# Kernel optimization log

Measured on AMD Instinct MI355X. Metric: run time of the kernel, lower is better.

The kernel has to match this reference:

```python
import jax, jax.numpy as jnp
import numpy as np

B, S, D, H = 2, 2048, 1024, 16
HD = D // H               # head_dim = input_size / num_heads
STEPS = 1                 # update_steps_max extra Hopfield update steps
LN_EPS = 1e-5
SCALING = 1.0 / np.sqrt(HD)  # beta = 1/sqrt(head_dim)


def layernorm(x, g, b):
    m = x.mean(-1, keepdims=True)
    v = ((x - m) ** 2).mean(-1, keepdims=True)
    return (x - m) * jax.lax.rsqrt(v + LN_EPS) * g + b


def setup_inputs() -> dict:
    key = jax.random.key(0)
    ks = jax.random.split(key, 9)
    s = 0.02
    f32 = jnp.float32
    return {
        "data": jax.random.normal(ks[0], (B, S, D), f32),
        # affine LayerNorm params (stored / state / projection patterns)
        "g_k": jnp.ones((D,), f32), "b_k": jnp.zeros((D,), f32),
        "g_q": jnp.ones((D,), f32), "b_q": jnp.zeros((D,), f32),
        "g_v": jnp.ones((D,), f32), "b_v": jnp.zeros((D,), f32),
        # in-projections (q/k/v) and out-projection of HopfieldCore
        "Wq": jax.random.normal(ks[1], (D, D), f32) * s, "bq": jnp.zeros((D,), f32),
        "Wk": jax.random.normal(ks[2], (D, D), f32) * s, "bk": jnp.zeros((D,), f32),
        "Wv": jax.random.normal(ks[3], (D, D), f32) * s, "bv": jnp.zeros((D,), f32),
        "Wo": jax.random.normal(ks[4], (D, D), f32) * s, "bo": jnp.zeros((D,), f32),
    }


def reference(data, g_k, b_k, g_q, b_q, g_v, b_v,
              Wq, bq, Wk, bk, Wv, bv, Wo, bo):
    # single input tensor used as stored / state / projection pattern
    xk = layernorm(data, g_k, b_k)   # stored pattern  -> keys
    xq = layernorm(data, g_q, b_q)   # state pattern   -> queries
    xv = layernorm(data, g_v, b_v)   # pattern proj    -> values

    split = lambda t: t.reshape(B, S, H, HD).transpose(0, 2, 1, 3)  # [B,H,S,HD]
    q = split(xq @ Wq + bq)
    k = split(xk @ Wk + bk)
    v = split(xv @ Wv + bv)

    def assoc(q):  # xi = softmax(beta * q K^T)
        return jax.nn.softmax(
            jnp.einsum('bhqd,bhkd->bhqk', q, k) * SCALING, axis=-1)

    xi = assoc(q)
    for _ in range(STEPS):           # iterative Hopfield update: q <- xi K
        q = jnp.einsum('bhqk,bhkd->bhqd', xi, k)
        xi = assoc(q)

    out = jnp.einsum('bhqk,bhkd->bhqd', xi, v)        # retrieve with values
    out = out.transpose(0, 2, 1, 3).reshape(B, S, D)  # merge heads
    return out @ Wo + bo
```

## Files before the change

kernel.cpp:

```cpp
#include <hip/hip_runtime.h>
#include <hip/hip_bf16.h>

#define B_  2
#define S_  2048
#define D_  1024
#define H_  16
#define HD_ 64
#define M_  4096


typedef __attribute__((ext_vector_type(8))) short short8;
typedef __attribute__((ext_vector_type(4))) float f32x4;

#define CE_ 0.1803368801111204f
#define SD_ 56

static __device__ __forceinline__ unsigned short f2bfc(float f){
  union{float f; unsigned u;} c; c.f = f;
  return (unsigned short)((c.u + 0x8000u) >> 16);
}
static __device__ __forceinline__ unsigned pk2bf(float a, float b){
  union{float f; unsigned u;} ca, cb; ca.f=a; cb.f=b;
  return __builtin_amdgcn_perm(cb.u + 0x8000u, ca.u + 0x8000u, 0x07060302u);
}
static __device__ __forceinline__ unsigned pk2bft(float a, float b){
  union{float f; unsigned u;} ca, cb; ca.f=a; cb.f=b;
  return __builtin_amdgcn_perm(cb.u, ca.u, 0x07060302u);
}

__global__ __launch_bounds__(256) void stats_kernel(const float* __restrict__ x,
                                                    float* __restrict__ mean,
                                                    float* __restrict__ rstd){
  int row = blockIdx.x*4 + (threadIdx.x>>6);
  int l = threadIdx.x & 63;
  const float4* xr = (const float4*)(x + (size_t)row*D_);
  float s = 0.f, ss = 0.f;
  #pragma unroll
  for (int i=0;i<4;i++){
    float4 v = xr[l + 64*i];
    s  += v.x+v.y+v.z+v.w;
    ss += v.x*v.x+v.y*v.y+v.z*v.z+v.w*v.w;
  }
  #pragma unroll
  for (int m=1;m<64;m<<=1){ s += __shfl_xor(s, m, 64); ss += __shfl_xor(ss, m, 64); }
  if (l==0){
    float me = s*(1.0f/D_);
    float var = ss*(1.0f/D_) - me*me;
    mean[row] = me;
    rstd[row] = rsqrtf(var + 1e-5f);
  }
}

__global__ __launch_bounds__(256) void biasfold_kernel(
  const float* __restrict__ Wq, const float* __restrict__ Wk, const float* __restrict__ Wv,
  const float* __restrict__ blq, const float* __restrict__ blk, const float* __restrict__ blv,
  const float* __restrict__ bpq, const float* __restrict__ bpk, const float* __restrict__ bpv,
  float* __restrict__ bf){
  int z = blockIdx.y;
  const float* W  = (z==0)?Wq:(z==1)?Wk:Wv;
  const float* bl = (z==0)?blq:(z==1)?blk:blv;
  const float* bp = (z==0)?bpq:(z==1)?bpk:bpv;
  int nl = threadIdx.x & 63, kg = threadIdx.x >> 6;
  int n = blockIdx.x*64 + nl;
  float acc = 0.f;
  for (int k = kg*256; k < (kg+1)*256; k++)
    acc += bl[k] * W[(size_t)k*D_ + n];
  __shared__ float red[4][64];
  red[kg][nl] = acc;
  __syncthreads();
  if (threadIdx.x < 64){
    int nn = blockIdx.x*64 + threadIdx.x;
    float v = red[0][threadIdx.x]+red[1][threadIdx.x]+red[2][threadIdx.x]+red[3][threadIdx.x]
              + bp[nn];
    bf[z*D_ + nn] = (z==0) ? v*CE_ : v;
  }
}

__global__ __launch_bounds__(256) void wtrans_kernel(
  const float* __restrict__ Wq, const float* __restrict__ Wk,
  const float* __restrict__ Wv, const float* __restrict__ Wo,
  const float* __restrict__ gq, const float* __restrict__ gk,
  const float* __restrict__ gv,
  unsigned short* __restrict__ WT){
  int z = blockIdx.z;
  const float* W = (z==0)?Wq:(z==1)?Wk:(z==2)?Wv:Wo;
  const float* g = (z==0)?gq:(z==1)?gk:(z==2)?gv:(const float*)0;
  unsigned short* out = WT + ((size_t)z<<20);
  int k0 = blockIdx.x*64, n0 = blockIdx.y*64;
  __shared__ unsigned short tile[64][72];
  int t = threadIdx.x;
  {
    int kr = t>>2, c16 = (t&3)*16;
    float gs = g ? g[k0+kr]*((z==0)?CE_:1.0f) : 1.0f;
    const float* src = W + (size_t)(k0+kr)*D_ + n0 + c16;
    float4 w0 = *(const float4*)(src);
    float4 w1 = *(const float4*)(src+4);
    float4 w2 = *(const float4*)(src+8);
    float4 w3 = *(const float4*)(src+12);
    unsigned* tp = (unsigned*)&tile[kr][c16];
    tp[0]=pk2bf(w0.x*gs,w0.y*gs); tp[1]=pk2bf(w0.z*gs,w0.w*gs);
    tp[2]=pk2bf(w1.x*gs,w1.y*gs); tp[3]=pk2bf(w1.z*gs,w1.w*gs);
    tp[4]=pk2bf(w2.x*gs,w2.y*gs); tp[5]=pk2bf(w2.z*gs,w2.w*gs);
    tp[6]=pk2bf(w3.x*gs,w3.y*gs); tp[7]=pk2bf(w3.z*gs,w3.w*gs);
  }
  __syncthreads();
  {
    int nr = t>>2, kc = (t&3)*16;
    union { uint4 v[2]; unsigned short u[16]; } st;
    #pragma unroll
    for (int i=0;i<16;i++) st.u[i] = tile[kc+i][nr];
    unsigned short* dst = out + (size_t)(n0+nr)*D_ + k0 + kc;
    *(uint4*)(dst)     = st.v[0];
    *(uint4*)(dst + 8) = st.v[1];
  }
}

__global__ __launch_bounds__(256) void gemm_qkv(
  const float* __restrict__ data,
  const unsigned short* __restrict__ WT,
  const float* __restrict__ biasf,
  const float* __restrict__ mean, const float* __restrict__ rstd,
  unsigned short* __restrict__ qv, unsigned short* __restrict__ kb,
  unsigned short* __restrict__ kT, unsigned short* __restrict__ vT)
{
  int z = blockIdx.z;
  const unsigned short* Bt = WT + ((size_t)z<<20);
  const float* bias = biasf + z*D_;
  unsigned short* oN = (z==0)?qv:(z==1)?kb:(unsigned short*)0;
  unsigned short* oT = (z==0)?(unsigned short*)0:(z==1)?kT:vT;

  __shared__ __align__(16) unsigned short As[128*SD_];
  __shared__ __align__(16) unsigned short Bs[128*SD_];
  int tid = threadIdx.x, w = tid>>6, l = tid&63;
  int m0 = blockIdx.x*128, n0 = blockIdx.y*128;
  int wr = (w>>1)*64, wc = (w&1)*64;
  int lr = l&15, qd = l>>4;
  int srow = tid>>2, scol = (tid&3)*8;

  float rs0 = rstd[m0+srow],    nm0 = -mean[m0+srow]*rs0;
  float rs1 = rstd[m0+srow+64], nm1 = -mean[m0+srow+64]*rs1;

  const f32x4 fz = {0.f,0.f,0.f,0.f};
  f32x4 acc[4][4];
  #pragma unroll
  for (int i=0;i<4;i++)
    #pragma unroll
    for (int j=0;j<4;j++) acc[i][j] = fz;

  for (int kk=0; kk<D_; kk+=32){
    __syncthreads();
    {
      const float* p0 = data + (size_t)(m0+srow   )*D_ + kk + scol;
      const float* p1 = data + (size_t)(m0+srow+64)*D_ + kk + scol;
      float4 a0 = *(const float4*)(p0), a0b = *(const float4*)(p0+4);
      float4 a1 = *(const float4*)(p1), a1b = *(const float4*)(p1+4);
      uint4 o0, o1;
      o0.x = pk2bf(fmaf(a0.x ,rs0,nm0), fmaf(a0.y ,rs0,nm0));
      o0.y = pk2bf(fmaf(a0.z ,rs0,nm0), fmaf(a0.w ,rs0,nm0));
      o0.z = pk2bf(fmaf(a0b.x,rs0,nm0), fmaf(a0b.y,rs0,nm0));
      o0.w = pk2bf(fmaf(a0b.z,rs0,nm0), fmaf(a0b.w,rs0,nm0));
      o1.x = pk2bf(fmaf(a1.x ,rs1,nm1), fmaf(a1.y ,rs1,nm1));
      o1.y = pk2bf(fmaf(a1.z ,rs1,nm1), fmaf(a1.w ,rs1,nm1));
      o1.z = pk2bf(fmaf(a1b.x,rs1,nm1), fmaf(a1b.y,rs1,nm1));
      o1.w = pk2bf(fmaf(a1b.z,rs1,nm1), fmaf(a1b.w,rs1,nm1));
      *(uint4*)(As + srow*SD_      + scol) = o0;
      *(uint4*)(As + (srow+64)*SD_ + scol) = o1;
    }
    *(uint4*)(Bs + srow*SD_      + scol) = *(const uint4*)(Bt + (size_t)(n0+srow   )*D_ + kk + scol);
    *(uint4*)(Bs + (srow+64)*SD_ + scol) = *(const uint4*)(Bt + (size_t)(n0+srow+64)*D_ + kk + scol);
    __syncthreads();
    short8 af[4], bfr[4];
    #pragma unroll
    for (int i=0;i<4;i++) af[i]  = *(const short8*)(As + (wr + i*16 + lr)*SD_ + qd*8);
    #pragma unroll
    for (int j=0;j<4;j++) bfr[j] = *(const short8*)(Bs + (wc + j*16 + lr)*SD_ + qd*8);
    #pragma unroll
    for (int i=0;i<4;i++)
      #pragma unroll
      for (int j=0;j<4;j++)
        acc[i][j] = __builtin_amdgcn_mfma_f32_16x16x32_bf16(af[i], bfr[j], acc[i][j], 0, 0, 0);
  }

  #pragma unroll
  for (int j=0;j<4;j++){
    int n = n0 + wc + j*16 + lr;
    float bias_n = bias[n];
    #pragma unroll
    for (int i=0;i<4;i++){
      int mb = m0 + wr + i*16 + qd*4;
      float v0 = acc[i][j][0] + bias_n;
      float v1 = acc[i][j][1] + bias_n;
      float v2 = acc[i][j][2] + bias_n;
      float v3 = acc[i][j][3] + bias_n;
      if (oN){
        oN[(size_t)(mb+0)*D_ + n] = f2bfc(v0);
        oN[(size_t)(mb+1)*D_ + n] = f2bfc(v1);
        oN[(size_t)(mb+2)*D_ + n] = f2bfc(v2);
        oN[(size_t)(mb+3)*D_ + n] = f2bfc(v3);
      }
      if (oT){
        int bb = mb >> 11, sI = mb & (S_-1);
        int hh = n >> 6,  dd = n & 63;
        uint2 pk; pk.x = pk2bf(v0, v1); pk.y = pk2bf(v2, v3);
        *(uint2*)(oT + (size_t)((bb*H_ + hh)*HD_ + dd)*S_ + sI) = pk;
      }
    }
  }
}

__global__ __launch_bounds__(256) void gemm_out(
  const unsigned short* __restrict__ A,
  const unsigned short* __restrict__ Bt,
  const float* __restrict__ bo,
  float* __restrict__ Cf)
{
  __shared__ __align__(16) unsigned short As[128*SD_];
  __shared__ __align__(16) unsigned short Bs[128*SD_];
  int tid = threadIdx.x, w = tid>>6, l = tid&63;
  int m0 = blockIdx.x*128, n0 = blockIdx.y*128;
  int wr = (w>>1)*64, wc = (w&1)*64;
  int lr = l&15, qd = l>>4;
  int srow = tid>>2, scol = (tid&3)*8;

  const f32x4 fz = {0.f,0.f,0.f,0.f};
  f32x4 acc[4][4];
  #pragma unroll
  for (int i=0;i<4;i++)
    #pragma unroll
    for (int j=0;j<4;j++) acc[i][j] = fz;

  for (int kk=0; kk<D_; kk+=32){
    __syncthreads();
    *(uint4*)(As + srow*SD_      + scol) = *(const uint4*)(A  + (size_t)(m0+srow   )*D_ + kk + scol);
    *(uint4*)(As + (srow+64)*SD_ + scol) = *(const uint4*)(A  + (size_t)(m0+srow+64)*D_ + kk + scol);
    *(uint4*)(Bs + srow*SD_      + scol) = *(const uint4*)(Bt + (size_t)(n0+srow   )*D_ + kk + scol);
    *(uint4*)(Bs + (srow+64)*SD_ + scol) = *(const uint4*)(Bt + (size_t)(n0+srow+64)*D_ + kk + scol);
    __syncthreads();
    short8 af[4], bfr[4];
    #pragma unroll
    for (int i=0;i<4;i++) af[i]  = *(const short8*)(As + (wr + i*16 + lr)*SD_ + qd*8);
    #pragma unroll
    for (int j=0;j<4;j++) bfr[j] = *(const short8*)(Bs + (wc + j*16 + lr)*SD_ + qd*8);
    #pragma unroll
    for (int i=0;i<4;i++)
      #pragma unroll
      for (int j=0;j<4;j++)
        acc[i][j] = __builtin_amdgcn_mfma_f32_16x16x32_bf16(af[i], bfr[j], acc[i][j], 0, 0, 0);
  }

  #pragma unroll
  for (int j=0;j<4;j++){
    int n = n0 + wc + j*16 + lr;
    float bias_n = bo[n];
    #pragma unroll
    for (int i=0;i<4;i++){
      int mb = m0 + wr + i*16 + qd*4;
      Cf[(size_t)(mb+0)*D_ + n] = acc[i][j][0] + bias_n;
      Cf[(size_t)(mb+1)*D_ + n] = acc[i][j][1] + bias_n;
      Cf[(size_t)(mb+2)*D_ + n] = acc[i][j][2] + bias_n;
      Cf[(size_t)(mb+3)*D_ + n] = acc[i][j][3] + bias_n;
    }
  }
}

__global__ __launch_bounds__(256) void attn_fused(
  unsigned short* __restrict__ QO,
  const unsigned short* __restrict__ K,
  const unsigned short* __restrict__ KT,
  const unsigned short* __restrict__ VT)
{
  int qt = blockIdx.x;
  int h  = blockIdx.y;
  int b  = qt >> 4;
  int bh = b*H_ + h;
  int tid = threadIdx.x, w = tid>>6, l = tid&63;
  int lr = l&15, qd = l>>4;
  int r8 = tid>>3, c8 = (tid&7)*8;
  int chf = c8>>5, co = c8&31;

  __shared__ __align__(16) unsigned short sK[2][64*SD_];
  __shared__ __align__(16) unsigned short sV[2][64*SD_];
  __shared__ __align__(16) unsigned short sP[4][2][32*SD_];

  const f32x4 fz = {0.f,0.f,0.f,0.f};

  unsigned short* Qbase = QO + (size_t)(qt*128 + w*32) * D_ + h*64;
  short8 qf[2][2];
  #pragma unroll
  for (int gg=0; gg<2; gg++)
    #pragma unroll
    for (int hf=0; hf<2; hf++)
      qf[gg][hf] = *(const short8*)(Qbase + (size_t)(gg*16+lr)*D_ + hf*32 + qd*8);

  const unsigned short* Khead = K + (size_t)(b*S_)*D_ + h*64;
  const unsigned short* Vh0 = KT + (size_t)bh*HD_*S_;
  const unsigned short* Vh1 = VT + (size_t)bh*HD_*S_;
  unsigned short* Pw0 = &sP[w][0][0];
  unsigned short* Pw1 = &sP[w][1][0];

  f32x4 oacc[2][4];
  float lac[2];

  uint4 kr0, kr1, vr0, vr1;
  {
    kr0 = *(const uint4*)(Khead + (size_t)(r8   )*D_ + c8);
    kr1 = *(const uint4*)(Khead + (size_t)(r8+32)*D_ + c8);
    vr0 = *(const uint4*)(Vh0 + (size_t)(r8   )*S_ + c8);
    vr1 = *(const uint4*)(Vh0 + (size_t)(r8+32)*S_ + c8);
  }

  #pragma unroll 1
  for (int phase=0; phase<2; phase++){
    const unsigned short* Vhead = phase ? Vh1 : Vh0;
    lac[0]=0.f; lac[1]=0.f;
    #pragma unroll
    for (int gg=0;gg<2;gg++)
      #pragma unroll
      for (int t=0;t<4;t++) oacc[gg][t]=fz;

    for (int kt=0; kt<S_; kt+=64){
      __syncthreads();
      *(uint4*)(&sK[chf][(r8   )*SD_ + co]) = kr0;
      *(uint4*)(&sK[chf][(r8+32)*SD_ + co]) = kr1;
      *(uint4*)(&sV[chf][(r8   )*SD_ + co]) = vr0;
      *(uint4*)(&sV[chf][(r8+32)*SD_ + co]) = vr1;
      __syncthreads();

      {
        int nkt = kt + 64;
        const unsigned short* Vn = Vhead;
        if (nkt >= S_){ nkt = 0; Vn = Vh1; }
        kr0 = *(const uint4*)(Khead + (size_t)(nkt+r8   )*D_ + c8);
        kr1 = *(const uint4*)(Khead + (size_t)(nkt+r8+32)*D_ + c8);
        vr0 = *(const uint4*)(Vn + (size_t)(r8   )*S_ + nkt + c8);
        vr1 = *(const uint4*)(Vn + (size_t)(r8+32)*S_ + nkt + c8);
      }

      f32x4 sc[2][4];
      #pragma unroll
      for (int st=0; st<4; st++){
        short8 kA0 = *(const short8*)(&sK[0][(st*16+lr)*SD_ + qd*8]);
        short8 kA1 = *(const short8*)(&sK[1][(st*16+lr)*SD_ + qd*8]);
        #pragma unroll
        for (int gg=0; gg<2; gg++){
          f32x4 z = fz;
          z = __builtin_amdgcn_mfma_f32_16x16x32_bf16(kA0, qf[gg][0], z, 0,0,0);
          z = __builtin_amdgcn_mfma_f32_16x16x32_bf16(kA1, qf[gg][1], z, 0,0,0);
          sc[gg][st] = z;
        }
      }
      #pragma unroll
      for (int gg=0; gg<2; gg++)
        #pragma unroll
        for (int st=0; st<4; st++){
          float p0=__builtin_amdgcn_exp2f(sc[gg][st][0]);
          float p1=__builtin_amdgcn_exp2f(sc[gg][st][1]);
          float p2=__builtin_amdgcn_exp2f(sc[gg][st][2]);
          float p3=__builtin_amdgcn_exp2f(sc[gg][st][3]);
          lac[gg] += (p0+p1)+(p2+p3);
          uint2 pk; pk.x = pk2bft(p0,p1); pk.y = pk2bft(p2,p3);
          unsigned short* Ph = (st&2) ? Pw1 : Pw0;
          *(uint2*)(Ph + (gg*16+lr)*SD_ + (st&1)*16 + qd*4) = pk;
        }
      short8 pf[2][2];
      #pragma unroll
      for (int gg=0; gg<2; gg++){
        pf[gg][0] = *(const short8*)(Pw0 + (gg*16+lr)*SD_ + qd*8);
        pf[gg][1] = *(const short8*)(Pw1 + (gg*16+lr)*SD_ + qd*8);
      }
      #pragma unroll
      for (int dt=0; dt<4; dt++){
        short8 vA0 = *(const short8*)(&sV[0][(dt*16+lr)*SD_ + qd*8]);
        short8 vA1 = *(const short8*)(&sV[1][(dt*16+lr)*SD_ + qd*8]);
        #pragma unroll
        for (int gg=0; gg<2; gg++){
          oacc[gg][dt] = __builtin_amdgcn_mfma_f32_16x16x32_bf16(vA0, pf[gg][0], oacc[gg][dt], 0,0,0);
          oacc[gg][dt] = __builtin_amdgcn_mfma_f32_16x16x32_bf16(vA1, pf[gg][1], oacc[gg][dt], 0,0,0);
        }
      }
    }

    #pragma unroll
    for (int gg=0;gg<2;gg++){
      lac[gg] += __shfl_xor(lac[gg], 16, 64);
      lac[gg] += __shfl_xor(lac[gg], 32, 64);
    }

    if (phase==0){
      #pragma unroll
      for (int gg=0;gg<2;gg++){
        float iv = CE_ * __builtin_amdgcn_rcpf(lac[gg]);
        #pragma unroll
        for (int dt=0;dt<4;dt++){
          uint2 pk;
          pk.x = pk2bf(oacc[gg][dt][0]*iv, oacc[gg][dt][1]*iv);
          pk.y = pk2bf(oacc[gg][dt][2]*iv, oacc[gg][dt][3]*iv);
          unsigned short* Ph = (dt&2) ? Pw1 : Pw0;
          *(uint2*)(Ph + (gg*16+lr)*SD_ + (dt&1)*16 + qd*4) = pk;
        }
      }
      __builtin_amdgcn_s_waitcnt(0);
      #pragma unroll
      for (int gg=0;gg<2;gg++){
        qf[gg][0] = *(const short8*)(Pw0 + (gg*16+lr)*SD_ + qd*8);
        qf[gg][1] = *(const short8*)(Pw1 + (gg*16+lr)*SD_ + qd*8);
      }
    } else {
      #pragma unroll
      for (int gg=0;gg<2;gg++){
        float iv = __builtin_amdgcn_rcpf(lac[gg]);
        unsigned short* Ob = QO + (size_t)(qt*128 + w*32 + gg*16 + lr)*D_ + h*64;
        #pragma unroll
        for (int dt=0;dt<4;dt++){
          uint2 pk;
          pk.x = pk2bf(oacc[gg][dt][0]*iv, oacc[gg][dt][1]*iv);
          pk.y = pk2bf(oacc[gg][dt][2]*iv, oacc[gg][dt][3]*iv);
          *(uint2*)(Ob + dt*16 + qd*4) = pk;
        }
      }
    }
  }
}

extern "C" void kernel_launch(void* const* d_in, const int* in_sizes, int n_in,
                              void* d_out, int out_size, void* d_ws, size_t ws_size,
                              hipStream_t stream){
  const float* data = (const float*)d_in[0];
  const float* g_k  = (const float*)d_in[1];
  const float* b_k  = (const float*)d_in[2];
  const float* g_q  = (const float*)d_in[3];
  const float* b_q  = (const float*)d_in[4];
  const float* g_v  = (const float*)d_in[5];
  const float* b_v  = (const float*)d_in[6];
  const float* Wq   = (const float*)d_in[7];
  const float* bq   = (const float*)d_in[8];
  const float* Wk   = (const float*)d_in[9];
  const float* bk   = (const float*)d_in[10];
  const float* Wv   = (const float*)d_in[11];
  const float* bv   = (const float*)d_in[12];
  const float* Wo   = (const float*)d_in[13];
  const float* bo   = (const float*)d_in[14];
  float* out = (float*)d_out;

  char* ws = (char*)d_ws;
  const size_t MB = (size_t)1<<20;
  unsigned short* q    = (unsigned short*)(ws);
  unsigned short* kb   = (unsigned short*)(ws + 8*MB);
  unsigned short* WT   = (unsigned short*)(ws + 16*MB);
  unsigned short* WTo  = WT + ((size_t)3<<20);
  float*          bfld = (float*)(ws + 24*MB);
  float*          mean = bfld + 3*D_;
  float*          rstd = mean + M_;
  unsigned short* vT   = (unsigned short*)d_out;
  unsigned short* kT   = (unsigned short*)((char*)d_out + 8*MB);

  dim3 gb(256);
  stats_kernel<<<dim3(M_/4), gb, 0, stream>>>(data, mean, rstd);
  biasfold_kernel<<<dim3(16,3), gb, 0, stream>>>(Wq,Wk,Wv, b_q,b_k,b_v, bq,bk,bv, bfld);
  wtrans_kernel<<<dim3(16,16,4), gb, 0, stream>>>(Wq,Wk,Wv,Wo, g_q,g_k,g_v, WT);
  gemm_qkv<<<dim3(32,8,3), gb, 0, stream>>>(data, WT, bfld, mean, rstd, q, kb, kT, vT);
  attn_fused<<<dim3(32, H_), gb, 0, stream>>>(q, kb, kT, vT);
  gemm_out<<<dim3(32,8), gb, 0, stream>>>(q, WTo, bo, out);
}
```

Baseline: 292.4 us.

## Merge prep kernels into one launch and use direct global-to-LDS loads in GEMMs

Three preprocessing kernels (row stats, weight transpose/convert, bias fold) are combined into one launch that dispatches on block index, removing two launch gaps. The QKV and output GEMMs now stage bf16 tiles with global_load_lds (direct global-to-LDS DMA) instead of going through registers, and those tiles use an unpadded 32-element row stride. The unpadded layout may bring back LDS bank conflicts on the fragment reads. The attention kernel, which likely dominates runtime, is not changed.

```diff
diff --git a/kernel.cpp b/kernel.cpp
--- a/kernel.cpp
+++ b/kernel.cpp
@@ -15,6 +15,12 @@
 #define CE_ 0.1803368801111204f
 #define SD_ 56
 
+typedef __attribute__((address_space(1))) const unsigned GU;
+typedef __attribute__((address_space(3))) unsigned LU;
+static __device__ __forceinline__ void glds16(const void* g, void* l){
+  __builtin_amdgcn_global_load_lds((GU*)g, (LU*)l, 16, 0, 0);
+}
+
 static __device__ __forceinline__ unsigned short f2bfc(float f){
   union{float f; unsigned u;} c; c.f = f;
   return (unsigned short)((c.u + 0x8000u) >> 16);
@@ -28,90 +34,86 @@
   return __builtin_amdgcn_perm(cb.u, ca.u, 0x07060302u);
 }
 
-__global__ __launch_bounds__(256) void stats_kernel(const float* __restrict__ x,
-                                                    float* __restrict__ mean,
-                                                    float* __restrict__ rstd){
-  int row = blockIdx.x*4 + (threadIdx.x>>6);
-  int l = threadIdx.x & 63;
-  const float4* xr = (const float4*)(x + (size_t)row*D_);
-  float s = 0.f, ss = 0.f;
-  #pragma unroll
-  for (int i=0;i<4;i++){
-    float4 v = xr[l + 64*i];
-    s  += v.x+v.y+v.z+v.w;
-    ss += v.x*v.x+v.y*v.y+v.z*v.z+v.w*v.w;
-  }
-  #pragma unroll
-  for (int m=1;m<64;m<<=1){ s += __shfl_xor(s, m, 64); ss += __shfl_xor(ss, m, 64); }
-  if (l==0){
-    float me = s*(1.0f/D_);
-    float var = ss*(1.0f/D_) - me*me;
-    mean[row] = me;
-    rstd[row] = rsqrtf(var + 1e-5f);
-  }
-}
-
-__global__ __launch_bounds__(256) void biasfold_kernel(
-  const float* __restrict__ Wq, const float* __restrict__ Wk, const float* __restrict__ Wv,
+__global__ __launch_bounds__(256) void prep_kernel(
+  const float* __restrict__ data, float* __restrict__ mean, float* __restrict__ rstd,
+  const float* __restrict__ Wq, const float* __restrict__ Wk,
+  const float* __restrict__ Wv, const float* __restrict__ Wo,
+  const float* __restrict__ gq, const float* __restrict__ gk, const float* __restrict__ gv,
   const float* __restrict__ blq, const float* __restrict__ blk, const float* __restrict__ blv,
   const float* __restrict__ bpq, const float* __restrict__ bpk, const float* __restrict__ bpv,
-  float* __restrict__ bf){
-  int z = blockIdx.y;
-  const float* W  = (z==0)?Wq:(z==1)?Wk:Wv;
-  const float* bl = (z==0)?blq:(z==1)?blk:blv;
-  const float* bp = (z==0)?bpq:(z==1)?bpk:bpv;
-  int nl = threadIdx.x & 63, kg = threadIdx.x >> 6;
-  int n = blockIdx.x*64 + nl;
-  float acc = 0.f;
-  for (int k = kg*256; k < (kg+1)*256; k++)
-    acc += bl[k] * W[(size_t)k*D_ + n];
+  unsigned short* __restrict__ WT, float* __restrict__ bf)
+{
+  __shared__ unsigned short tile[64][72];
   __shared__ float red[4][64];
-  red[kg][nl] = acc;
-  __syncthreads();
-  if (threadIdx.x < 64){
-    int nn = blockIdx.x*64 + threadIdx.x;
-    float v = red[0][threadIdx.x]+red[1][threadIdx.x]+red[2][threadIdx.x]+red[3][threadIdx.x]
-              + bp[nn];
-    bf[z*D_ + nn] = (z==0) ? v*CE_ : v;
-  }
-}
-
-__global__ __launch_bounds__(256) void wtrans_kernel(
-  const float* __restrict__ Wq, const float* __restrict__ Wk,
-  const float* __restrict__ Wv, const float* __restrict__ Wo,
-  const float* __restrict__ gq, const float* __restrict__ gk,
-  const float* __restrict__ gv,
-  unsigned short* __restrict__ WT){
-  int z = blockIdx.z;
-  const float* W = (z==0)?Wq:(z==1)?Wk:(z==2)?Wv:Wo;
-  const float* g = (z==0)?gq:(z==1)?gk:(z==2)?gv:(const float*)0;
-  unsigned short* out = WT + ((size_t)z<<20);
-  int k0 = blockIdx.x*64, n0 = blockIdx.y*64;
-  __shared__ unsigned short tile[64][72];
-  int t = threadIdx.x;
-  {
-    int kr = t>>2, c16 = (t&3)*16;
-    float gs = g ? g[k0+kr]*((z==0)?CE_:1.0f) : 1.0f;
-    const float* src = W + (size_t)(k0+kr)*D_ + n0 + c16;
-    float4 w0 = *(const float4*)(src);
-    float4 w1 = *(const float4*)(src+4);
-    float4 w2 = *(const float4*)(src+8);
-    float4 w3 = *(const float4*)(src+12);
-    unsigned* tp = (unsigned*)&tile[kr][c16];
-    tp[0]=pk2bf(w0.x*gs,w0.y*gs); tp[1]=pk2bf(w0.z*gs,w0.w*gs);
-    tp[2]=pk2bf(w1.x*gs,w1.y*gs); tp[3]=pk2bf(w1.z*gs,w1.w*gs);
-    tp[4]=pk2bf(w2.x*gs,w2.y*gs); tp[5]=pk2bf(w2.z*gs,w2.w*gs);
-    tp[6]=pk2bf(w3.x*gs,w3.y*gs); tp[7]=pk2bf(w3.z*gs,w3.w*gs);
-  }
-  __syncthreads();
-  {
-    int nr = t>>2, kc = (t&3)*16;
-    union { uint4 v[2]; unsigned short u[16]; } st;
-    #pragma unroll
-    for (int i=0;i<16;i++) st.u[i] = tile[kc+i][nr];
-    unsigned short* dst = out + (size_t)(n0+nr)*D_ + k0 + kc;
-    *(uint4*)(dst)     = st.v[0];
-    *(uint4*)(dst + 8) = st.v[1];
+  int bid = blockIdx.x, t = threadIdx.x;
+  if (bid < 1024){
+    int row = bid*4 + (t>>6);
+    int l = t & 63;
+    const float4* xr = (const float4*)(data + (size_t)row*D_);
+    float s = 0.f, ss = 0.f;
+    #pragma unroll
+    for (int i=0;i<4;i++){
+      float4 v = xr[l + 64*i];
+      s  += v.x+v.y+v.z+v.w;
+      ss += v.x*v.x+v.y*v.y+v.z*v.z+v.w*v.w;
+    }
+    #pragma unroll
+    for (int m=1;m<64;m<<=1){ s += __shfl_xor(s, m, 64); ss += __shfl_xor(ss, m, 64); }
+    if (l==0){
+      float me = s*(1.0f/D_);
+      float var = ss*(1.0f/D_) - me*me;
+      mean[row] = me;
+      rstd[row] = rsqrtf(var + 1e-5f);
+    }
+  } else if (bid < 2048){
+    int idx = bid - 1024;
+    int z = idx >> 8, rem = idx & 255;
+    int k0 = (rem>>4)*64, n0 = (rem&15)*64;
+    const float* W = (z==0)?Wq:(z==1)?Wk:(z==2)?Wv:Wo;
+    const float* g = (z==0)?gq:(z==1)?gk:(z==2)?gv:(const float*)0;
+    unsigned short* out = WT + ((size_t)z<<20);
+    {
+      int kr = t>>2, c16 = (t&3)*16;
+      float gs = g ? g[k0+kr]*((z==0)?CE_:1.0f) : 1.0f;
+      const float* src = W + (size_t)(k0+kr)*D_ + n0 + c16;
+      float4 w0 = *(const float4*)(src);
+      float4 w1 = *(const float4*)(src+4);
+      float4 w2 = *(const float4*)(src+8);
+      float4 w3 = *(const float4*)(src+12);
+      unsigned* tp = (unsigned*)&tile[kr][c16];
+      tp[0]=pk2bf(w0.x*gs,w0.y*gs); tp[1]=pk2bf(w0.z*gs,w0.w*gs);
+      tp[2]=pk2bf(w1.x*gs,w1.y*gs); tp[3]=pk2bf(w1.z*gs,w1.w*gs);
+      tp[4]=pk2bf(w2.x*gs,w2.y*gs); tp[5]=pk2bf(w2.z*gs,w2.w*gs);
+      tp[6]=pk2bf(w3.x*gs,w3.y*gs); tp[7]=pk2bf(w3.z*gs,w3.w*gs);
+    }
+    __syncthreads();
+    {
+      int nr = t>>2, kc = (t&3)*16;
+      union { uint4 v[2]; unsigned short u[16]; } st;
+      #pragma unroll
+      for (int i=0;i<16;i++) st.u[i] = tile[kc+i][nr];
+      unsigned short* dst = out + (size_t)(n0+nr)*D_ + k0 + kc;
+      *(uint4*)(dst)     = st.v[0];
+      *(uint4*)(dst + 8) = st.v[1];
+    }
+  } else {
+    int idx = bid - 2048;
+    int z = idx >> 4, xb = idx & 15;
+    const float* W  = (z==0)?Wq:(z==1)?Wk:Wv;
+    const float* bl = (z==0)?blq:(z==1)?blk:blv;
+    const float* bp = (z==0)?bpq:(z==1)?bpk:bpv;
+    int nl = t & 63, kg = t >> 6;
+    int n = xb*64 + nl;
+    float acc = 0.f;
+    for (int k = kg*256; k < (kg+1)*256; k++)
+      acc += bl[k] * W[(size_t)k*D_ + n];
+    red[kg][nl] = acc;
+    __syncthreads();
+    if (t < 64){
+      int nn = xb*64 + t;
+      float v = red[0][t]+red[1][t]+red[2][t]+red[3][t] + bp[nn];
+      bf[z*D_ + nn] = (z==0) ? v*CE_ : v;
+    }
   }
 }
 
@@ -130,7 +132,7 @@
   unsigned short* oT = (z==0)?(unsigned short*)0:(z==1)?kT:vT;
 
   __shared__ __align__(16) unsigned short As[128*SD_];
-  __shared__ __align__(16) unsigned short Bs[128*SD_];
+  __shared__ __align__(16) unsigned short Bs[128*32];
   int tid = threadIdx.x, w = tid>>6, l = tid&63;
   int m0 = blockIdx.x*128, n0 = blockIdx.y*128;
   int wr = (w>>1)*64, wc = (w&1)*64;
@@ -140,6 +142,10 @@
   float rs0 = rstd[m0+srow],    nm0 = -mean[m0+srow]*rs0;
   float rs1 = rstd[m0+srow+64], nm1 = -mean[m0+srow+64]*rs1;
 
+  const unsigned short* gB = Bt + (size_t)(n0 + w*32 + (l>>2))*D_ + (l&3)*8;
+  unsigned short* lB0 = &Bs[(w*32)*32];
+  unsigned short* lB1 = &Bs[(w*32+16)*32];
+
   const f32x4 fz = {0.f,0.f,0.f,0.f};
   f32x4 acc[4][4];
   #pragma unroll
@@ -149,6 +155,8 @@
 
   for (int kk=0; kk<D_; kk+=32){
     __syncthreads();
+    glds16(gB + kk,                 lB0);
+    glds16(gB + kk + (size_t)16*D_, lB1);
     {
       const float* p0 = data + (size_t)(m0+srow   )*D_ + kk + scol;
       const float* p1 = data + (size_t)(m0+srow+64)*D_ + kk + scol;
@@ -166,14 +174,12 @@
       *(uint4*)(As + srow*SD_      + scol) = o0;
       *(uint4*)(As + (srow+64)*SD_ + scol) = o1;
     }
-    *(uint4*)(Bs + srow*SD_      + scol) = *(const uint4*)(Bt + (size_t)(n0+srow   )*D_ + kk + scol);
-    *(uint4*)(Bs + (srow+64)*SD_ + scol) = *(const uint4*)(Bt + (size_t)(n0+srow+64)*D_ + kk + scol);
     __syncthreads();
     short8 af[4], bfr[4];
     #pragma unroll
     for (int i=0;i<4;i++) af[i]  = *(const short8*)(As + (wr + i*16 + lr)*SD_ + qd*8);
     #pragma unroll
-    for (int j=0;j<4;j++) bfr[j] = *(const short8*)(Bs + (wc + j*16 + lr)*SD_ + qd*8);
+    for (int j=0;j<4;j++) bfr[j] = *(const short8*)(Bs + (wc + j*16 + lr)*32 + qd*8);
     #pragma unroll
     for (int i=0;i<4;i++)
       #pragma unroll
@@ -214,13 +220,19 @@
   const float* __restrict__ bo,
   float* __restrict__ Cf)
 {
-  __shared__ __align__(16) unsigned short As[128*SD_];
-  __shared__ __align__(16) unsigned short Bs[128*SD_];
+  __shared__ __align__(16) unsigned short As[128*32];
+  __shared__ __align__(16) unsigned short Bs[128*32];
   int tid = threadIdx.x, w = tid>>6, l = tid&63;
   int m0 = blockIdx.x*128, n0 = blockIdx.y*128;
   int wr = (w>>1)*64, wc = (w&1)*64;
   int lr = l&15, qd = l>>4;
-  int srow = tid>>2, scol = (tid&3)*8;
+
+  const unsigned short* gA = A  + (size_t)(m0 + w*32 + (l>>2))*D_ + (l&3)*8;
+  const unsigned short* gB = Bt + (size_t)(n0 + w*32 + (l>>2))*D_ + (l&3)*8;
+  unsigned short* lA0 = &As[(w*32)*32];
+  unsigned short* lA1 = &As[(w*32+16)*32];
+  unsigned short* lB0 = &Bs[(w*32)*32];
+  unsigned short* lB1 = &Bs[(w*32+16)*32];
 
   const f32x4 fz = {0.f,0.f,0.f,0.f};
   f32x4 acc[4][4];
@@ -231,16 +243,16 @@
 
   for (int kk=0; kk<D_; kk+=32){
     __syncthreads();
-    *(uint4*)(As + srow*SD_      + scol) = *(const uint4*)(A  + (size_t)(m0+srow   )*D_ + kk + scol);
-    *(uint4*)(As + (srow+64)*SD_ + scol) = *(const uint4*)(A  + (size_t)(m0+srow+64)*D_ + kk + scol);
-    *(uint4*)(Bs + srow*SD_      + scol) = *(const uint4*)(Bt + (size_t)(n0+srow   )*D_ + kk + scol);
-    *(uint4*)(Bs + (srow+64)*SD_ + scol) = *(const uint4*)(Bt + (size_t)(n0+srow+64)*D_ + kk + scol);
+    glds16(gA + kk,                 lA0);
+    glds16(gA + kk + (size_t)16*D_, lA1);
+    glds16(gB + kk,                 lB0);
+    glds16(gB + kk + (size_t)16*D_, lB1);
     __syncthreads();
     short8 af[4], bfr[4];
     #pragma unroll
-    for (int i=0;i<4;i++) af[i]  = *(const short8*)(As + (wr + i*16 + lr)*SD_ + qd*8);
-    #pragma unroll
-    for (int j=0;j<4;j++) bfr[j] = *(const short8*)(Bs + (wc + j*16 + lr)*SD_ + qd*8);
+    for (int i=0;i<4;i++) af[i]  = *(const short8*)(As + (wr + i*16 + lr)*32 + qd*8);
+    #pragma unroll
+    for (int j=0;j<4;j++) bfr[j] = *(const short8*)(Bs + (wc + j*16 + lr)*32 + qd*8);
     #pragma unroll
     for (int i=0;i<4;i++)
       #pragma unroll
@@ -455,9 +467,9 @@
   unsigned short* kT   = (unsigned short*)((char*)d_out + 8*MB);
 
   dim3 gb(256);
-  stats_kernel<<<dim3(M_/4), gb, 0, stream>>>(data, mean, rstd);
-  biasfold_kernel<<<dim3(16,3), gb, 0, stream>>>(Wq,Wk,Wv, b_q,b_k,b_v, bq,bk,bv, bfld);
-  wtrans_kernel<<<dim3(16,16,4), gb, 0, stream>>>(Wq,Wk,Wv,Wo, g_q,g_k,g_v, WT);
+  prep_kernel<<<dim3(2096), gb, 0, stream>>>(data, mean, rstd,
+                                             Wq, Wk, Wv, Wo, g_q, g_k, g_v,
+                                             b_q, b_k, b_v, bq, bk, bv, WT, bfld);
   gemm_qkv<<<dim3(32,8,3), gb, 0, stream>>>(data, WT, bfld, mean, rstd, q, kb, kT, vT);
   attn_fused<<<dim3(32, H_), gb, 0, stream>>>(q, kb, kT, vT);
   gemm_out<<<dim3(32,8), gb, 0, stream>>>(q, WTo, bo, out);
```

New measurement: 276.9 us. 5.3% less time.
